# Kernel optimization log

Hardware: AMD Instinct MI355X
Metric: run time of the kernel (lower is better)

Reference implementation:

```python
import jax, jax.numpy as jnp
import numpy as np

L = 3        # num_layers
B = 8192     # batch slots
H = 1024     # hidden_dim (== decoder_in_dim)
D_IN = 1024
D_OUT = 80
N_ACT = 4096 # active rows selected by hidden_idx


def setup_inputs() -> dict:
    key = jax.random.key(0)
    ks = jax.random.split(key, 8)
    encoded = jax.random.normal(ks[0], (B, D_IN), jnp.float32)
    hidden = jax.random.normal(ks[1], (L, B, H), jnp.float32)
    hidden_idx = jnp.arange(N_ACT, dtype=jnp.int32)  # unique, in-range batch indices
    s = 0.05  # small init scale for stable gate math
    w_ih = jax.random.normal(ks[2], (L, 3 * H, D_IN), jnp.float32) * s
    w_hh = jax.random.normal(ks[3], (L, 3 * H, H), jnp.float32) * s
    b_ih = jax.random.normal(ks[4], (L, 3 * H), jnp.float32) * s
    b_hh = jax.random.normal(ks[5], (L, 3 * H), jnp.float32) * s
    w_out = jax.random.normal(ks[6], (D_OUT, H), jnp.float32) * s
    b_out = jax.random.normal(ks[7], (D_OUT,), jnp.float32) * s
    return {"encoded": encoded, "hidden": hidden, "hidden_idx": hidden_idx,
            "w_ih": w_ih, "w_hh": w_hh, "b_ih": b_ih, "b_hh": b_hh,
            "w_out": w_out, "b_out": b_out}


def reference(encoded, hidden, hidden_idx, w_ih, w_hh, b_ih, b_hh, w_out, b_out):
    # Gather active rows, run stacked GRUCells, scatter back (eval mode: dropout = identity).
    x = encoded[hidden_idx]                       # [N, D_IN]
    new_hidden = []
    for i in range(L):                            # small fixed layer loop
        h_full = hidden[i]                        # [B, H]
        h = h_full[hidden_idx]                    # [N, H]
        gi = x @ w_ih[i].T + b_ih[i]              # [N, 3H] gates from input
        gh = h @ w_hh[i].T + b_hh[i]              # [N, 3H] gates from hidden
        i_r, i_z, i_n = jnp.split(gi, 3, axis=-1)
        h_r, h_z, h_n = jnp.split(gh, 3, axis=-1)
        r = jax.nn.sigmoid(i_r + h_r)
        z = jax.nn.sigmoid(i_z + h_z)
        n = jnp.tanh(i_n + r * h_n)
        h_out = (1.0 - z) * n + z * h             # torch GRUCell update
        x = h_out
        new_hidden.append(h_full.at[hidden_idx].set(h_out))
    y = jnp.tanh(x @ w_out.T + b_out)             # linear head + tanh activation
    output = jnp.zeros((B, D_OUT), y.dtype).at[hidden_idx].set(y)
    return (output, jnp.stack(new_hidden))
```

## Files before the change

kernel.cpp:

```cpp
#include <hip/hip_runtime.h>

typedef unsigned short ushort_t;
typedef unsigned char uchar_t;
typedef unsigned int uint_t;
typedef __attribute__((ext_vector_type(8))) short bf16x8;
typedef __attribute__((ext_vector_type(4))) float f32x4;

constexpr int L_   = 3;
constexpr int B_   = 8192;
constexpr int H_   = 1024;
constexpr int DOUT_= 80;
constexpr int NACT_= 4096;
constexpr int G3_  = 3 * H_;

static __device__ __forceinline__ ushort_t f2bf(float f) {
    uint_t u = __float_as_uint(f);
    uint_t r = (u + 0x7FFFu + ((u >> 16) & 1u)) >> 16;
    return (ushort_t)r;
}

static __device__ __forceinline__ void gll16(const void* g, void* l) {
    __builtin_amdgcn_global_load_lds(
        (const __attribute__((address_space(1))) uint32_t*)g,
        (__attribute__((address_space(3))) uint32_t*)l, 16, 0, 0);
}

__global__ void prep_all(const float* __restrict__ encoded, const float* __restrict__ hidden,
                         const int* __restrict__ idx,
                         const float* __restrict__ wih, const float* __restrict__ whh,
                         const float* __restrict__ wout,
                         ushort_t* __restrict__ oih, ushort_t* __restrict__ ohh,
                         ushort_t* __restrict__ oout,
                         ushort_t* __restrict__ x0, ushort_t* __restrict__ hb,
                         uchar_t* __restrict__ mask) {
    int tid = blockIdx.x * blockDim.x + threadIdx.x;
    int nth = gridDim.x * blockDim.x;
    if (tid < NACT_) mask[idx[tid]] = 1;
    const int NW = L_ * G3_ * H_ / 4;
    for (int i = tid; i < NW; i += nth) {
        float4 a = ((const float4*)wih)[i];
        ushort4 o; o.x = f2bf(a.x); o.y = f2bf(a.y); o.z = f2bf(a.z); o.w = f2bf(a.w);
        ((ushort4*)oih)[i] = o;
        float4 b = ((const float4*)whh)[i];
        ushort4 p; p.x = f2bf(b.x); p.y = f2bf(b.y); p.z = f2bf(b.z); p.w = f2bf(b.w);
        ((ushort4*)ohh)[i] = p;
    }
    const int NO = DOUT_ * H_ / 4;
    for (int i = tid; i < NO; i += nth) {
        float4 a = ((const float4*)wout)[i];
        ushort4 o; o.x = f2bf(a.x); o.y = f2bf(a.y); o.z = f2bf(a.z); o.w = f2bf(a.w);
        ((ushort4*)oout)[i] = o;
    }
    const int C4 = H_ / 4;
    const int PER = NACT_ * C4;
    for (int i = tid; i < 4 * PER; i += nth) {
        int seg = i / PER;
        int rem = i - seg * PER;
        int r = rem / C4, c = rem % C4;
        int gr = idx[r];
        const float* src = (seg == 0) ? (encoded + (size_t)gr * H_)
                                      : (hidden + ((size_t)(seg - 1) * B_ + gr) * H_);
        float4 v = ((const float4*)src)[c];
        ushort4 o; o.x = f2bf(v.x); o.y = f2bf(v.y); o.z = f2bf(v.z); o.w = f2bf(v.w);
        ushort_t* dst = (seg == 0) ? x0 : (hb + (size_t)(seg - 1) * NACT_ * H_);
        ((ushort4*)(dst + (size_t)r * H_))[c] = o;
    }
}

__global__ void copy_inactive(const float* __restrict__ hidden, const uchar_t* __restrict__ mask,
                              float* __restrict__ outh) {
    const int total = L_ * B_ * (H_ / 4);
    int i = blockIdx.x * blockDim.x + threadIdx.x;
    int nth = gridDim.x * blockDim.x;
    for (; i < total; i += nth) {
        int row = (i >> 8) & (B_ - 1);
        if (mask[row]) continue;
        ((float4*)outh)[i] = ((const float4*)hidden)[i];
    }
}

template<bool LAST>
static __device__ __forceinline__ void gru_sweep(
    const ushort_t* __restrict__ cA, const ushort_t* __restrict__ cW,
    const ushort_t* __restrict__ nA, const ushort_t* __restrict__ nW,
    const uint_t* aoff, const uint_t* woff,
    ushort_t* lds0, ushort_t* lds1,
    int wave, int wr, int wc, int fl, int fh,
    f32x4 (&accR)[4][2], f32x4 (&accZ)[4][2], f32x4 (&accN)[4][2])
{
#pragma unroll 2
    for (int kki = 0; kki < 16; ++kki) {
        ushort_t* rb = (kki & 1) ? lds1 : lds0;
        ushort_t* sb = (kki & 1) ? lds0 : lds1;
        if (kki < 15) {
#pragma unroll
            for (int t = 0; t < 4; ++t) gll16(cA + aoff[t] + (kki + 1) * 64, sb + wave * 2048 + t * 512);
#pragma unroll
            for (int t = 0; t < 6; ++t) gll16(cW + woff[t] + (kki + 1) * 64, sb + 8192 + wave * 3072 + t * 512);
            asm volatile("s_waitcnt vmcnt(10)" ::: "memory");
        } else if (!LAST) {
#pragma unroll
            for (int t = 0; t < 4; ++t) gll16(nA + aoff[t], sb + wave * 2048 + t * 512);
#pragma unroll
            for (int t = 0; t < 6; ++t) gll16(nW + woff[t], sb + 8192 + wave * 3072 + t * 512);
            asm volatile("s_waitcnt vmcnt(10)" ::: "memory");
        } else {
            asm volatile("s_waitcnt vmcnt(0)" ::: "memory");
        }
        __builtin_amdgcn_s_barrier();
        asm volatile("" ::: "memory");
        __builtin_amdgcn_sched_barrier(0);
#pragma unroll
        for (int ks = 0; ks < 2; ++ks) {
            const int sl = ((ks * 4 + fh) ^ (fl & 7)) * 8;
            bf16x8 a[4];
#pragma unroll
            for (int m = 0; m < 4; ++m)
                a[m] = *(const bf16x8*)&rb[(wr * 64 + m * 16 + fl) * 64 + sl];
#pragma unroll
            for (int g = 0; g < 3; ++g) {
#pragma unroll
                for (int n = 0; n < 2; ++n) {
                    const bf16x8 b = *(const bf16x8*)&rb[8192 + (g * 64 + wc * 32 + n * 16 + fl) * 64 + sl];
#pragma unroll
                    for (int m = 0; m < 4; ++m) {
                        if (g == 0)
                            accR[m][n] = __builtin_amdgcn_mfma_f32_16x16x32_bf16(a[m], b, accR[m][n], 0, 0, 0);
                        else if (g == 1)
                            accZ[m][n] = __builtin_amdgcn_mfma_f32_16x16x32_bf16(a[m], b, accZ[m][n], 0, 0, 0);
                        else
                            accN[m][n] = __builtin_amdgcn_mfma_f32_16x16x32_bf16(a[m], b, accN[m][n], 0, 0, 0);
                    }
                }
            }
        }
        __builtin_amdgcn_sched_barrier(0);
        __builtin_amdgcn_s_barrier();
    }
}

__global__ __launch_bounds__(256, 2) void gru_layer(
    const ushort_t* __restrict__ xb,
    const ushort_t* __restrict__ hb,
    const float* __restrict__ hid_full,
    const ushort_t* __restrict__ wih,
    const ushort_t* __restrict__ whh,
    const float* __restrict__ bih, const float* __restrict__ bhh,
    const int* __restrict__ idx,
    float* __restrict__ out_hid,
    ushort_t* __restrict__ xnext)
{
    __shared__ ushort_t lds[2][20480];

    const int tid = threadIdx.x;
    const int bid = blockIdx.x;
    const int swz = (bid & 7) * 64 + (bid >> 3);
    const int bn = swz & 15, bm = swz >> 4;
    const int row0 = bm * 128, col0 = bn * 64;
    const int wave = tid >> 6, lane = tid & 63;
    const int wr = wave >> 1, wc = wave & 1;
    const int fl = lane & 15, fh = lane >> 4;
    const int srow = lane >> 3;
    const int sxor = ((lane & 7) ^ srow) * 8;

    uint_t aoff[4], woff[6];
#pragma unroll
    for (int t = 0; t < 4; ++t)
        aoff[t] = (uint_t)(row0 + wave * 32 + t * 8 + srow) * H_ + sxor;
#pragma unroll
    for (int t = 0; t < 6; ++t) {
        const int slot = wave * 48 + t * 8 + srow;
        woff[t] = (uint_t)((slot >> 6) * H_ + col0 + (slot & 63)) * H_ + sxor;
    }

    f32x4 accR[4][2] = {};
    f32x4 accZ[4][2] = {};
    f32x4 accNx[4][2] = {};
    f32x4 accNh[4][2] = {};

#pragma unroll
    for (int t = 0; t < 4; ++t) gll16(xb + aoff[t], lds[0] + wave * 2048 + t * 512);
#pragma unroll
    for (int t = 0; t < 6; ++t) gll16(wih + woff[t], lds[0] + 8192 + wave * 3072 + t * 512);

    gru_sweep<false>(xb, wih, hb, whh, aoff, woff, lds[0], lds[1],
                     wave, wr, wc, fl, fh, accR, accZ, accNx);
    gru_sweep<true >(hb, whh, nullptr, nullptr, aoff, woff, lds[0], lds[1],
                     wave, wr, wc, fl, fh, accR, accZ, accNh);

#pragma unroll
    for (int m = 0; m < 4; ++m) {
#pragma unroll
        for (int n = 0; n < 2; ++n) {
            const int c = col0 + wc * 32 + n * 16 + fl;
            const float br_r = bih[c] + bhh[c];
            const float br_z = bih[H_ + c] + bhh[H_ + c];
            const float bi_n = bih[2 * H_ + c];
            const float bh_n = bhh[2 * H_ + c];
#pragma unroll
            for (int j = 0; j < 4; ++j) {
                const int r = row0 + wr * 64 + m * 16 + fh * 4 + j;
                const float vr = 1.f / (1.f + expf(-(accR[m][n][j] + br_r)));
                const float vz = 1.f / (1.f + expf(-(accZ[m][n][j] + br_z)));
                const float vn = tanhf(accNx[m][n][j] + bi_n + vr * (accNh[m][n][j] + bh_n));
                const int gr = idx[r];
                const float h0 = hid_full[(size_t)gr * H_ + c];
                const float ho = (1.f - vz) * vn + vz * h0;
                out_hid[(size_t)gr * H_ + c] = ho;
                xnext[(size_t)r * H_ + c] = f2bf(ho);
            }
        }
    }
}

__global__ __launch_bounds__(256) void head_gemm(
    const ushort_t* __restrict__ xb, const ushort_t* __restrict__ wo,
    const float* __restrict__ bo, const int* __restrict__ idx,
    float* __restrict__ outy)
{
    __shared__ ushort_t Xs[64][72];
    __shared__ ushort_t Ws[80][72];
    const int tid = threadIdx.x;
    const int row0 = blockIdx.x * 64;
    const int lrow = tid >> 2, lseg = tid & 3;
    const int wave = tid >> 6, lane = tid & 63;
    const int fl = lane & 15, fh = lane >> 4;
    f32x4 acc[5] = {};

    for (int kk = 0; kk < H_; kk += 64) {
        __syncthreads();
        const ushort_t* xp = xb + (size_t)(row0 + lrow) * H_ + kk + lseg * 16;
        *(uint4*)&Xs[lrow][lseg * 16]     = *(const uint4*)xp;
        *(uint4*)&Xs[lrow][lseg * 16 + 8] = *(const uint4*)(xp + 8);
        for (int t = tid; t < 320; t += 256) {
            int r = t >> 2, s = t & 3;
            const ushort_t* wp = wo + (size_t)r * H_ + kk + s * 16;
            *(uint4*)&Ws[r][s * 16]     = *(const uint4*)wp;
            *(uint4*)&Ws[r][s * 16 + 8] = *(const uint4*)(wp + 8);
        }
        __syncthreads();
#pragma unroll
        for (int ks = 0; ks < 64; ks += 32) {
            bf16x8 a = *(const bf16x8*)&Xs[wave * 16 + fl][ks + fh * 8];
#pragma unroll
            for (int nf = 0; nf < 5; ++nf) {
                bf16x8 b = *(const bf16x8*)&Ws[nf * 16 + fl][ks + fh * 8];
                acc[nf] = __builtin_amdgcn_mfma_f32_16x16x32_bf16(a, b, acc[nf], 0, 0, 0);
            }
        }
    }
#pragma unroll
    for (int nf = 0; nf < 5; ++nf) {
        const int c = nf * 16 + fl;
        const float bb = bo[c];
#pragma unroll
        for (int j = 0; j < 4; ++j) {
            const int r = row0 + wave * 16 + fh * 4 + j;
            const float y = tanhf(acc[nf][j] + bb);
            outy[(size_t)idx[r] * DOUT_ + c] = y;
        }
    }
}

extern "C" void kernel_launch(void* const* d_in, const int* in_sizes, int n_in,
                              void* d_out, int out_size, void* d_ws, size_t ws_size,
                              hipStream_t stream) {
    const float* encoded = (const float*)d_in[0];
    const float* hidden  = (const float*)d_in[1];
    const int*   idx     = (const int*)d_in[2];
    const float* w_ih    = (const float*)d_in[3];
    const float* w_hh    = (const float*)d_in[4];
    const float* b_ih    = (const float*)d_in[5];
    const float* b_hh    = (const float*)d_in[6];
    const float* w_out   = (const float*)d_in[7];
    const float* b_out   = (const float*)d_in[8];

    float* outy = (float*)d_out;
    float* outh = outy + (size_t)B_ * DOUT_;

    ushort_t* ws    = (ushort_t*)d_ws;
    ushort_t* wihb  = ws;
    ushort_t* whhb  = wihb + (size_t)L_ * G3_ * H_;
    ushort_t* woutb = whhb + (size_t)L_ * G3_ * H_;
    ushort_t* xb0   = woutb + (size_t)DOUT_ * H_;
    ushort_t* xb1   = xb0 + (size_t)NACT_ * H_;
    ushort_t* hb    = xb1 + (size_t)NACT_ * H_;
    uchar_t*  mask  = (uchar_t*)(hb + (size_t)L_ * NACT_ * H_);

    hipMemsetAsync(outy, 0, (size_t)B_ * DOUT_ * sizeof(float), stream);
    hipMemsetAsync(mask, 0, B_, stream);
    prep_all<<<2048, 256, 0, stream>>>(encoded, hidden, idx, w_ih, w_hh, w_out,
                                       wihb, whhb, woutb, xb0, hb, mask);
    copy_inactive<<<2048, 256, 0, stream>>>(hidden, mask, outh);

    ushort_t* xin = xb0;
    ushort_t* xout = xb1;
    for (int i = 0; i < L_; ++i) {
        gru_layer<<<512, 256, 0, stream>>>(
            xin, hb + (size_t)i * NACT_ * H_, hidden + (size_t)i * B_ * H_,
            wihb + (size_t)i * G3_ * H_, whhb + (size_t)i * G3_ * H_,
            b_ih + (size_t)i * G3_, b_hh + (size_t)i * G3_, idx,
            outh + (size_t)i * B_ * H_, xout);
        ushort_t* t = xin; xin = xout; xout = t;
    }
    head_gemm<<<64, 256, 0, stream>>>(xin, woutb, b_out, idx, outy);
}
```

Before: 279.1 us.

## Triple-buffer GRU GEMM pipeline as single 32-stage loop with MFMA priority

Replaces the two separate double-buffered K sweeps with one 32-stage loop over both the input and hidden GEMMs, using three LDS buffers so loads run two stages ahead. It also preloads all B fragments before issuing MFMAs and raises wave priority around the MFMA block. The third buffer raises LDS use to about 120KB, so launch bounds drop to one block per CU. That trades occupancy for deeper prefetch and removes the second barrier per iteration.

```diff
diff --git a/kernel.cpp b/kernel.cpp
--- a/kernel.cpp
+++ b/kernel.cpp
@@ -24,6 +24,8 @@
         (const __attribute__((address_space(1))) uint32_t*)g,
         (__attribute__((address_space(3))) uint32_t*)l, 16, 0, 0);
 }
+
+#define MFMA16(A, B, C) __builtin_amdgcn_mfma_f32_16x16x32_bf16((A), (B), (C), 0, 0, 0)
 
 __global__ void prep_all(const float* __restrict__ encoded, const float* __restrict__ hidden,
                          const int* __restrict__ idx,
@@ -79,67 +81,7 @@
     }
 }
 
-template<bool LAST>
-static __device__ __forceinline__ void gru_sweep(
-    const ushort_t* __restrict__ cA, const ushort_t* __restrict__ cW,
-    const ushort_t* __restrict__ nA, const ushort_t* __restrict__ nW,
-    const uint_t* aoff, const uint_t* woff,
-    ushort_t* lds0, ushort_t* lds1,
-    int wave, int wr, int wc, int fl, int fh,
-    f32x4 (&accR)[4][2], f32x4 (&accZ)[4][2], f32x4 (&accN)[4][2])
-{
-#pragma unroll 2
-    for (int kki = 0; kki < 16; ++kki) {
-        ushort_t* rb = (kki & 1) ? lds1 : lds0;
-        ushort_t* sb = (kki & 1) ? lds0 : lds1;
-        if (kki < 15) {
-#pragma unroll
-            for (int t = 0; t < 4; ++t) gll16(cA + aoff[t] + (kki + 1) * 64, sb + wave * 2048 + t * 512);
-#pragma unroll
-            for (int t = 0; t < 6; ++t) gll16(cW + woff[t] + (kki + 1) * 64, sb + 8192 + wave * 3072 + t * 512);
-            asm volatile("s_waitcnt vmcnt(10)" ::: "memory");
-        } else if (!LAST) {
-#pragma unroll
-            for (int t = 0; t < 4; ++t) gll16(nA + aoff[t], sb + wave * 2048 + t * 512);
-#pragma unroll
-            for (int t = 0; t < 6; ++t) gll16(nW + woff[t], sb + 8192 + wave * 3072 + t * 512);
-            asm volatile("s_waitcnt vmcnt(10)" ::: "memory");
-        } else {
-            asm volatile("s_waitcnt vmcnt(0)" ::: "memory");
-        }
-        __builtin_amdgcn_s_barrier();
-        asm volatile("" ::: "memory");
-        __builtin_amdgcn_sched_barrier(0);
-#pragma unroll
-        for (int ks = 0; ks < 2; ++ks) {
-            const int sl = ((ks * 4 + fh) ^ (fl & 7)) * 8;
-            bf16x8 a[4];
-#pragma unroll
-            for (int m = 0; m < 4; ++m)
-                a[m] = *(const bf16x8*)&rb[(wr * 64 + m * 16 + fl) * 64 + sl];
-#pragma unroll
-            for (int g = 0; g < 3; ++g) {
-#pragma unroll
-                for (int n = 0; n < 2; ++n) {
-                    const bf16x8 b = *(const bf16x8*)&rb[8192 + (g * 64 + wc * 32 + n * 16 + fl) * 64 + sl];
-#pragma unroll
-                    for (int m = 0; m < 4; ++m) {
-                        if (g == 0)
-                            accR[m][n] = __builtin_amdgcn_mfma_f32_16x16x32_bf16(a[m], b, accR[m][n], 0, 0, 0);
-                        else if (g == 1)
-                            accZ[m][n] = __builtin_amdgcn_mfma_f32_16x16x32_bf16(a[m], b, accZ[m][n], 0, 0, 0);
-                        else
-                            accN[m][n] = __builtin_amdgcn_mfma_f32_16x16x32_bf16(a[m], b, accN[m][n], 0, 0, 0);
-                    }
-                }
-            }
-        }
-        __builtin_amdgcn_sched_barrier(0);
-        __builtin_amdgcn_s_barrier();
-    }
-}
-
-__global__ __launch_bounds__(256, 2) void gru_layer(
+__global__ __launch_bounds__(256, 1) void gru_layer(
     const ushort_t* __restrict__ xb,
     const ushort_t* __restrict__ hb,
     const float* __restrict__ hid_full,
@@ -150,7 +92,7 @@
     float* __restrict__ out_hid,
     ushort_t* __restrict__ xnext)
 {
-    __shared__ ushort_t lds[2][20480];
+    __shared__ ushort_t lds[3][20480];
 
     const int tid = threadIdx.x;
     const int bid = blockIdx.x;
@@ -173,30 +115,78 @@
         woff[t] = (uint_t)((slot >> 6) * H_ + col0 + (slot & 63)) * H_ + sxor;
     }
 
-    f32x4 accR[4][2] = {};
-    f32x4 accZ[4][2] = {};
-    f32x4 accNx[4][2] = {};
-    f32x4 accNh[4][2] = {};
-
-#pragma unroll
-    for (int t = 0; t < 4; ++t) gll16(xb + aoff[t], lds[0] + wave * 2048 + t * 512);
-#pragma unroll
-    for (int t = 0; t < 6; ++t) gll16(wih + woff[t], lds[0] + 8192 + wave * 3072 + t * 512);
-
-    gru_sweep<false>(xb, wih, hb, whh, aoff, woff, lds[0], lds[1],
-                     wave, wr, wc, fl, fh, accR, accZ, accNx);
-    gru_sweep<true >(hb, whh, nullptr, nullptr, aoff, woff, lds[0], lds[1],
-                     wave, wr, wc, fl, fh, accR, accZ, accNh);
-
-#pragma unroll
-    for (int m = 0; m < 4; ++m) {
-#pragma unroll
-        for (int n = 0; n < 2; ++n) {
-            const int c = col0 + wc * 32 + n * 16 + fl;
-            const float br_r = bih[c] + bhh[c];
-            const float br_z = bih[H_ + c] + bhh[H_ + c];
-            const float bi_n = bih[2 * H_ + c];
-            const float bh_n = bhh[2 * H_ + c];
+    f32x4 accR[4][2] = {}, accZ[4][2] = {}, accNx[4][2] = {}, accNh[4][2] = {};
+
+#define STAGE(t, buf)                                                              \
+    do {                                                                           \
+        const ushort_t* A_ = ((t) < 16) ? xb : hb;                                 \
+        const ushort_t* W_ = ((t) < 16) ? wih : whh;                               \
+        const int k_ = ((t) & 15) * 64;                                            \
+        _Pragma("unroll")                                                          \
+        for (int i_ = 0; i_ < 4; ++i_)                                             \
+            gll16(A_ + aoff[i_] + k_, (buf) + wave * 2048 + i_ * 512);             \
+        _Pragma("unroll")                                                          \
+        for (int i_ = 0; i_ < 6; ++i_)                                             \
+            gll16(W_ + woff[i_] + k_, (buf) + 8192 + wave * 3072 + i_ * 512);      \
+    } while (0)
+
+    STAGE(0, &lds[0][0]);
+    STAGE(1, &lds[1][0]);
+
+    ushort_t* b0 = &lds[0][0];
+    ushort_t* b1 = &lds[1][0];
+    ushort_t* b2 = &lds[2][0];
+
+    for (int s = 0; s < 32; ++s) {
+        if (s < 30) {
+            STAGE(s + 2, b2);
+            asm volatile("s_waitcnt vmcnt(20)" ::: "memory");
+        } else if (s == 30) {
+            asm volatile("s_waitcnt vmcnt(10)" ::: "memory");
+        } else {
+            asm volatile("s_waitcnt vmcnt(0)" ::: "memory");
+        }
+        __builtin_amdgcn_s_barrier();
+        asm volatile("" ::: "memory");
+        const bool isX = (s < 16);
+#pragma unroll
+        for (int ks = 0; ks < 2; ++ks) {
+            const int sl = ((ks * 4 + fh) ^ (fl & 7)) * 8;
+            bf16x8 a[4];
+#pragma unroll
+            for (int m = 0; m < 4; ++m)
+                a[m] = *(const bf16x8*)&b0[(wr * 64 + m * 16 + fl) * 64 + sl];
+            bf16x8 b[3][2];
+#pragma unroll
+            for (int g = 0; g < 3; ++g)
+#pragma unroll
+                for (int n = 0; n < 2; ++n)
+                    b[g][n] = *(const bf16x8*)&b0[8192 + (g * 64 + wc * 32 + n * 16 + fl) * 64 + sl];
+            __builtin_amdgcn_s_setprio(1);
+#pragma unroll
+            for (int n = 0; n < 2; ++n)
+#pragma unroll
+                for (int m = 0; m < 4; ++m) {
+                    accR[m][n] = MFMA16(a[m], b[0][n], accR[m][n]);
+                    accZ[m][n] = MFMA16(a[m], b[1][n], accZ[m][n]);
+                    if (isX) accNx[m][n] = MFMA16(a[m], b[2][n], accNx[m][n]);
+                    else     accNh[m][n] = MFMA16(a[m], b[2][n], accNh[m][n]);
+                }
+            __builtin_amdgcn_s_setprio(0);
+        }
+        ushort_t* tb = b0; b0 = b1; b1 = b2; b2 = tb;
+    }
+#undef STAGE
+
+#pragma unroll
+    for (int n = 0; n < 2; ++n) {
+        const int c = col0 + wc * 32 + n * 16 + fl;
+        const float br_r = bih[c] + bhh[c];
+        const float br_z = bih[H_ + c] + bhh[H_ + c];
+        const float bi_n = bih[2 * H_ + c];
+        const float bh_n = bhh[2 * H_ + c];
+#pragma unroll
+        for (int m = 0; m < 4; ++m) {
 #pragma unroll
             for (int j = 0; j < 4; ++j) {
                 const int r = row0 + wr * 64 + m * 16 + fh * 4 + j;
@@ -245,7 +235,7 @@
 #pragma unroll
             for (int nf = 0; nf < 5; ++nf) {
                 bf16x8 b = *(const bf16x8*)&Ws[nf * 16 + fl][ks + fh * 8];
-                acc[nf] = __builtin_amdgcn_mfma_f32_16x16x32_bf16(a, b, acc[nf], 0, 0, 0);
+                acc[nf] = MFMA16(a, b, acc[nf]);
             }
         }
     }
```

Measured after the change: 408.3 us. +46.3%, slower.
